# Optimization experiments

Hardware: AMD Instinct MI355X
Metric: run time of the kernel (lower is better)

Reference implementation:

```python
import jax, jax.numpy as jnp
import numpy as np

B, S, DIM = 2, 2048, 2048
H, KVH, HD = 16, 4, 128
WIN = 512
ROPE_BASE = 10000.0
EPS = 1.1920928955078125e-07  # torch F.rms_norm default eps for fp32


def setup_inputs() -> dict:
    key = jax.random.key(0)
    ks = jax.random.split(key, 6)
    kv_dim = KVH * HD
    sc = lambda fan_in: 1.0 / np.sqrt(fan_in)
    return {
        "x": jax.random.normal(ks[0], (B, S, DIM), jnp.float32),
        "Wq": jax.random.normal(ks[1], (DIM, DIM), jnp.float32) * sc(DIM),
        "Wk": jax.random.normal(ks[2], (kv_dim, DIM), jnp.float32) * sc(DIM),
        "Wv": jax.random.normal(ks[3], (kv_dim, DIM), jnp.float32) * sc(DIM),
        "Wo": jax.random.normal(ks[4], (DIM, DIM), jnp.float32) * sc(DIM),
        "q_gain": jnp.ones((H,), jnp.float32),
    }


def _rms_norm(x):
    return x * jax.lax.rsqrt(jnp.mean(x * x, axis=-1, keepdims=True) + EPS)


def _rope_tables(seqlen, dtype):
    half = HD // 2
    inv_freq = ROPE_BASE ** (-jnp.arange(0, half, dtype=jnp.float32) / half)
    freqs = jnp.arange(seqlen, dtype=jnp.float32)[:, None] * inv_freq[None, :]  # [S, HD/2]
    return jnp.cos(freqs).astype(dtype), jnp.sin(freqs).astype(dtype)


def _apply_rotary(x, cos, sin):
    # x: [B, H, S, HD]; cos/sin: [S, HD/2]
    half = x.shape[-1] // 2
    x1, x2 = x[..., :half], x[..., half:]
    c = cos[None, None, :, :]
    s = sin[None, None, :, :]
    return jnp.concatenate([x1 * c + x2 * s, -x1 * s + x2 * c], axis=-1)


def reference(x, Wq, Wk, Wv, Wo, q_gain):
    bsz, seqlen, dim = x.shape
    q = jnp.einsum("bsd,ed->bse", x, Wq).reshape(bsz, seqlen, H, HD).transpose(0, 2, 1, 3)
    k = jnp.einsum("bsd,ed->bse", x, Wk).reshape(bsz, seqlen, KVH, HD).transpose(0, 2, 1, 3)
    v = jnp.einsum("bsd,ed->bse", x, Wv).reshape(bsz, seqlen, KVH, HD).transpose(0, 2, 1, 3)

    q = _rms_norm(q)
    k = _rms_norm(k)

    cos, sin = _rope_tables(seqlen, q.dtype)
    q = _apply_rotary(q, cos, sin)
    k = _apply_rotary(k, cos, sin)

    q = q * q_gain[None, :, None, None]

    # GQA: expand kv heads to match query heads
    rep = H // KVH
    k = jnp.repeat(k, rep, axis=1)
    v = jnp.repeat(v, rep, axis=1)

    row = jnp.arange(seqlen)[:, None]
    col = jnp.arange(seqlen)[None, :]
    mask = (col <= row) & (col >= row - WIN + 1)  # [S, S]

    scale = 1.0 / np.sqrt(HD)
    scores = jnp.einsum("bhsd,bhtd->bhst", q, k) * scale
    scores = jnp.where(mask[None, None, :, :], scores, -jnp.inf)
    attn = jax.nn.softmax(scores, axis=-1)
    y = jnp.einsum("bhst,bhtd->bhsd", attn, v)  # [B, H, S, HD]

    y = y.transpose(0, 2, 1, 3).reshape(bsz, seqlen, dim)
    return jnp.einsum("bsd,ed->bse", y, Wo)
```

## Files before the change

### kernel.cpp

```cpp
#include <hip/hip_runtime.h>

#define S_LEN 2048
#define DIM   2048
#define NH    16
#define NKV   4
#define HD    128
#define WIN   512
#define BATCH 2

typedef __bf16 bf16x8 __attribute__((ext_vector_type(8)));
typedef __bf16 bf16x4 __attribute__((ext_vector_type(4)));
typedef float  f32x4  __attribute__((ext_vector_type(4)));

__device__ inline void async_load16(const void* g, void* l) {
  __builtin_amdgcn_global_load_lds(
      (const __attribute__((address_space(1))) unsigned int*)g,
      (__attribute__((address_space(3))) unsigned int*)l, 16, 0, 0);
}

__global__ __launch_bounds__(256) void rope_tables_kernel(
    float* __restrict__ cosT, float* __restrict__ sinT) {
  int idx = blockIdx.x * 256 + threadIdx.x;
  int s = idx >> 6, d = idx & 63;
  float f = (float)s * powf(10000.f, -(float)d * (1.f / 64.f));
  float sn, cs;
  sincosf(f, &sn, &cs);
  cosT[idx] = cs;
  sinT[idx] = sn;
}

__global__ __launch_bounds__(256) void cast_bf16_kernel(
    const float* __restrict__ in, __bf16* __restrict__ out, int n4) {
  int i = blockIdx.x * 256 + threadIdx.x;
  if (i < n4) {
    float4 v = ((const float4*)in)[i];
    bf16x4 o;
    o[0] = (__bf16)v.x; o[1] = (__bf16)v.y; o[2] = (__bf16)v.z; o[3] = (__bf16)v.w;
    ((bf16x4*)out)[i] = o;
  }
}

__global__ __launch_bounds__(256) void cast_weights_kernel(
    const float* __restrict__ Wq, const float* __restrict__ Wk,
    const float* __restrict__ Wv, const float* __restrict__ Wo,
    __bf16* __restrict__ wqkv, __bf16* __restrict__ wob) {
  int i = blockIdx.x * 256 + threadIdx.x;
  int orow = i >> 9, c = i & 511;
  const float* src;
  __bf16* dst;
  long soff;
  if (orow < 2048) {
    int n = orow & 127;
    int sr = (orow & ~127) + ((n >> 5) << 4) + (n & 15) + (((n >> 4) & 1) << 6);
    src = Wq; soff = (long)sr * 512 + c; dst = wqkv + (long)orow * 2048;
  } else if (orow < 2560) {
    int lr = orow - 2048, n = lr & 127;
    int sr = (lr & ~127) + ((n >> 5) << 4) + (n & 15) + (((n >> 4) & 1) << 6);
    src = Wk; soff = (long)sr * 512 + c; dst = wqkv + (long)orow * 2048;
  } else if (orow < 3072) {
    src = Wv; soff = (long)(orow - 2560) * 512 + c; dst = wqkv + (long)orow * 2048;
  } else {
    src = Wo; soff = (long)(orow - 3072) * 512 + c; dst = wob + (long)(orow - 3072) * 2048;
  }
  float4 v = ((const float4*)src)[soff];
  bf16x4 o;
  o[0] = (__bf16)v.x; o[1] = (__bf16)v.y; o[2] = (__bf16)v.z; o[3] = (__bf16)v.w;
  ((bf16x4*)(dst))[c] = o;
}

__global__ __launch_bounds__(256) void gemm_bt(
    const __bf16* __restrict__ A, const __bf16* __restrict__ Bt,
    float* __restrict__ C, int M, int N, int K) {
  __shared__ __bf16 As[128 * 32];
  __shared__ __bf16 Bs[128 * 32];
  const int t = threadIdx.x;
  const int wid = t >> 6, lane = t & 63;
  const int quad = lane >> 4, l15 = lane & 15;
  const long m0 = (long)blockIdx.x * 128, n0 = (long)blockIdx.y * 128;
  const int wm = (wid >> 1) * 64, wn = (wid & 1) * 64;

  const __bf16* ga = A + (m0 + (t >> 2)) * (long)K + (t & 3) * 8;
  const __bf16* gb = Bt + (n0 + (t >> 2)) * (long)K + (t & 3) * 8;
  char* lA = (char*)As + wid * 1024;
  char* lB = (char*)Bs + wid * 1024;
  const long rstride = 64L * K;

  f32x4 zero = {0.f, 0.f, 0.f, 0.f};
  f32x4 acc[4][4];
#pragma unroll
  for (int i = 0; i < 4; ++i)
#pragma unroll
    for (int j = 0; j < 4; ++j) acc[i][j] = zero;

  for (int k0 = 0; k0 < K; k0 += 32) {
    async_load16(ga + k0, lA);
    async_load16(ga + k0 + rstride, lA + 4096);
    async_load16(gb + k0, lB);
    async_load16(gb + k0 + rstride, lB + 4096);
    __syncthreads();
    bf16x8 af[4], bfr[4];
#pragma unroll
    for (int i = 0; i < 4; ++i) {
      af[i] = *(const bf16x8*)(As + (wm + i * 16 + l15) * 32 + quad * 8);
      bfr[i] = *(const bf16x8*)(Bs + (wn + i * 16 + l15) * 32 + quad * 8);
    }
#pragma unroll
    for (int i = 0; i < 4; ++i)
#pragma unroll
      for (int j = 0; j < 4; ++j)
        acc[i][j] = __builtin_amdgcn_mfma_f32_16x16x32_bf16(af[i], bfr[j], acc[i][j], 0, 0, 0);
    __syncthreads();
  }

#pragma unroll
  for (int i = 0; i < 4; ++i)
#pragma unroll
    for (int j = 0; j < 4; ++j)
#pragma unroll
      for (int r = 0; r < 4; ++r)
        C[(m0 + wm + i * 16 + quad * 4 + r) * (long)N + n0 + wn + j * 16 + l15] = acc[i][j][r];
}

__global__ __launch_bounds__(256) void gemm_qkv(
    const __bf16* __restrict__ A,
    const __bf16* __restrict__ Bt,
    const float* __restrict__ gain,
    const float* __restrict__ cosT, const float* __restrict__ sinT,
    __bf16* __restrict__ Qo,
    __bf16* __restrict__ Ko,
    __bf16* __restrict__ Vt) {
  __shared__ __bf16 As[128 * 32];
  __shared__ __bf16 Bs[128 * 32];
  const int K = 2048;
  const int t = threadIdx.x;
  const int wid = t >> 6, lane = t & 63;
  const int quad = lane >> 4, l15 = lane & 15;
  const long m0 = (long)blockIdx.x * 128, n0 = (long)blockIdx.y * 128;
  const int wm = (wid >> 1) * 64, wn = (wid & 1) * 64;

  const __bf16* ga = A + (m0 + (t >> 2)) * (long)K + (t & 3) * 8;
  const __bf16* gb = Bt + (n0 + (t >> 2)) * (long)K + (t & 3) * 8;
  char* lA = (char*)As + wid * 1024;
  char* lB = (char*)Bs + wid * 1024;
  const long rstride = 64L * K;

  f32x4 zero = {0.f, 0.f, 0.f, 0.f};
  f32x4 acc[4][4];
#pragma unroll
  for (int i = 0; i < 4; ++i)
#pragma unroll
    for (int j = 0; j < 4; ++j) acc[i][j] = zero;

  for (int k0 = 0; k0 < K; k0 += 32) {
    async_load16(ga + k0, lA);
    async_load16(ga + k0 + rstride, lA + 4096);
    async_load16(gb + k0, lB);
    async_load16(gb + k0 + rstride, lB + 4096);
    __syncthreads();
    bf16x8 af[4], bfr[4];
#pragma unroll
    for (int i = 0; i < 4; ++i) {
      af[i] = *(const bf16x8*)(As + (wm + i * 16 + l15) * 32 + quad * 8);
      bfr[i] = *(const bf16x8*)(Bs + (wn + i * 16 + l15) * 32 + quad * 8);
    }
#pragma unroll
    for (int i = 0; i < 4; ++i)
#pragma unroll
      for (int j = 0; j < 4; ++j)
        acc[i][j] = __builtin_amdgcn_mfma_f32_16x16x32_bf16(af[i], bfr[j], acc[i][j], 0, 0, 0);
    __syncthreads();
  }

  const int by = blockIdx.y;
  const int srow0 = (int)(m0 & 2047);
  const int bb = (int)(m0 >> 11);

  if (by >= 20) {
    const int kvh = by - 20;
    __bf16* Vb = Vt + ((long)(bb * NKV + kvh)) * HD * S_LEN;
#pragma unroll
    for (int i = 0; i < 4; ++i)
#pragma unroll
      for (int j = 0; j < 4; ++j) {
        int d = wn + j * 16 + l15;
        int s0 = srow0 + wm + i * 16 + quad * 4;
        bf16x4 o;
#pragma unroll
        for (int r = 0; r < 4; ++r) o[r] = (__bf16)acc[i][j][r];
        *(bf16x4*)(Vb + (long)d * S_LEN + s0) = o;
      }
  } else {
    float* sums = (float*)As;
#pragma unroll
    for (int i = 0; i < 4; ++i)
#pragma unroll
      for (int r = 0; r < 4; ++r) {
        float t2 = acc[i][0][r] * acc[i][0][r] + acc[i][1][r] * acc[i][1][r] +
                   acc[i][2][r] * acc[i][2][r] + acc[i][3][r] * acc[i][3][r];
#pragma unroll
        for (int off = 1; off < 16; off <<= 1) t2 += __shfl_xor(t2, off, 64);
        if (l15 == 0) sums[(wm + i * 16 + quad * 4 + r) * 2 + (wn >> 6)] = t2;
      }
    __syncthreads();

    float g;
    __bf16* base;
    if (by < 16) {
      g = gain[by] * 0.08838834764831845f;
      base = Qo + ((long)(bb * NH + by)) * S_LEN * HD;
    } else {
      g = 1.f;
      base = Ko + ((long)(bb * NKV + (by - 16))) * S_LEN * HD;
    }
#pragma unroll
    for (int i = 0; i < 4; ++i)
#pragma unroll
      for (int r = 0; r < 4; ++r) {
        int lrow = wm + i * 16 + quad * 4 + r;
        int srow = srow0 + lrow;
        float rs = rsqrtf((sums[lrow * 2] + sums[lrow * 2 + 1]) * (1.f / 128.f) +
                          1.1920928955078125e-07f);
#pragma unroll
        for (int a = 0; a < 2; ++a) {
          int dlow = (wn >> 1) + a * 16 + l15;
          float cv = cosT[srow * 64 + dlow];
          float sv = sinT[srow * 64 + dlow];
          float x1 = acc[i][2 * a][r] * rs;
          float x2 = acc[i][2 * a + 1][r] * rs;
          base[(long)srow * HD + wn + (2 * a) * 16 + l15] = (__bf16)((x1 * cv + x2 * sv) * g);
          base[(long)srow * HD + wn + (2 * a + 1) * 16 + l15] = (__bf16)((-x1 * sv + x2 * cv) * g);
        }
      }
  }
}

__global__ __launch_bounds__(128) void attn_kernel(
    const __bf16* __restrict__ Q,
    const __bf16* __restrict__ K,
    const __bf16* __restrict__ Vt,
    const float* __restrict__ gain,
    __bf16* __restrict__ Y) {
  __shared__ __bf16 Ks[64 * 128];
  __shared__ __bf16 Vs[128 * 64];
  __shared__ __bf16 Ps[2][32 * 64];

  const int t = threadIdx.x;
  const int wid = t >> 6, lane = t & 63;
  const int quad = lane >> 4, l15 = lane & 15;
  const int qt = 31 - blockIdx.x;
  const int h = blockIdx.y, b = blockIdx.z;
  const int kv = h >> 2;
  const int t0 = qt * 64;
  const int r0 = t0 + wid * 32;

  const __bf16* Qb = Q + ((long)(b * NH + h)) * S_LEN * HD;
  const __bf16* Kb = K + ((long)(b * NKV + kv)) * S_LEN * HD;
  const __bf16* Vb = Vt + ((long)(b * NKV + kv)) * HD * S_LEN;
  const float M = 11.3137085f * fabsf(gain[h]);

  bf16x8 qf[2][4];
#pragma unroll
  for (int mt = 0; mt < 2; ++mt)
#pragma unroll
    for (int c = 0; c < 4; ++c)
      qf[mt][c] = *(const bf16x8*)(Qb + (long)(r0 + mt * 16 + l15) * HD + c * 32 + quad * 8);

  f32x4 zero = {0.f, 0.f, 0.f, 0.f};
  f32x4 acc[2][8];
#pragma unroll
  for (int mt = 0; mt < 2; ++mt)
#pragma unroll
    for (int d = 0; d < 8; ++d) acc[mt][d] = zero;
  float lac[2][4];
#pragma unroll
  for (int mt = 0; mt < 2; ++mt)
#pragma unroll
    for (int r = 0; r < 4; ++r) lac[mt][r] = 0.f;

  int koff[8], voff[8];
#pragma unroll
  for (int jj = 0; jj < 8; ++jj) {
    int kr = wid * 32 + jj * 4 + (lane >> 4);
    koff[jj] = kr * HD + (((lane & 15) ^ (kr & 7)) << 3);
    int vr = wid * 64 + jj * 8 + (lane >> 3);
    voff[jj] = vr * S_LEN + (((lane & 7) ^ (vr & 7)) << 3);
  }

  const int kstart = (t0 >= WIN) ? (t0 - WIN) : 0;
  const int ntiles = (t0 + 64 - kstart) >> 6;

  for (int it = 0; it < ntiles; ++it) {
    const int kt = kstart + it * 64;
#pragma unroll
    for (int jj = 0; jj < 8; ++jj) {
      async_load16(Kb + (long)kt * HD + koff[jj], (char*)Ks + wid * 8192 + jj * 1024);
      async_load16(Vb + kt + voff[jj], (char*)Vs + wid * 8192 + jj * 1024);
    }
    __syncthreads();

    if (kt <= r0 + 31 && kt + 63 >= r0 - (WIN - 1)) {
      f32x4 sc[2][4];
#pragma unroll
      for (int nt = 0; nt < 4; ++nt) { sc[0][nt] = zero; sc[1][nt] = zero; }
#pragma unroll
      for (int nt = 0; nt < 4; ++nt)
#pragma unroll
        for (int c = 0; c < 4; ++c) {
          bf16x8 kf = *(const bf16x8*)(Ks + (nt * 16 + l15) * 128 +
                                       (((c * 4 + quad) ^ (l15 & 7)) << 3));
          sc[0][nt] = __builtin_amdgcn_mfma_f32_16x16x32_bf16(qf[0][c], kf, sc[0][nt], 0, 0, 0);
          sc[1][nt] = __builtin_amdgcn_mfma_f32_16x16x32_bf16(qf[1][c], kf, sc[1][nt], 0, 0, 0);
        }
#pragma unroll
      for (int mt = 0; mt < 2; ++mt)
#pragma unroll
        for (int r = 0; r < 4; ++r) {
          const int prow = mt * 16 + quad * 4 + r;
          const int row = r0 + prow;
#pragma unroll
          for (int nt = 0; nt < 4; ++nt) {
            const int key = kt + nt * 16 + l15;
            float p = (key <= row && key >= row - (WIN - 1))
                          ? __expf(sc[mt][nt][r] - M) : 0.f;
            lac[mt][r] += p;
            int chunk = nt * 2 + (l15 >> 3);
            Ps[wid][prow * 64 + ((chunk ^ (prow & 7)) << 3) + (l15 & 7)] = (__bf16)p;
          }
        }
      bf16x8 pf[2][2];
#pragma unroll
      for (int mt = 0; mt < 2; ++mt)
#pragma unroll
        for (int kc = 0; kc < 2; ++kc)
          pf[mt][kc] = *(const bf16x8*)(&Ps[wid][(mt * 16 + l15) * 64 +
                                                 (((kc * 4 + quad) ^ (l15 & 7)) << 3)]);
#pragma unroll
      for (int dt = 0; dt < 8; ++dt)
#pragma unroll
        for (int kc = 0; kc < 2; ++kc) {
          bf16x8 vf = *(const bf16x8*)(Vs + (dt * 16 + l15) * 64 +
                                       (((kc * 4 + quad) ^ (l15 & 7)) << 3));
          acc[0][dt] = __builtin_amdgcn_mfma_f32_16x16x32_bf16(pf[0][kc], vf, acc[0][dt], 0, 0, 0);
          acc[1][dt] = __builtin_amdgcn_mfma_f32_16x16x32_bf16(pf[1][kc], vf, acc[1][dt], 0, 0, 0);
        }
    }
    __syncthreads();
  }

  __bf16* Yb = Y + ((long)b * S_LEN) * DIM + h * HD;
#pragma unroll
  for (int mt = 0; mt < 2; ++mt)
#pragma unroll
    for (int r = 0; r < 4; ++r) {
      float ls = lac[mt][r];
#pragma unroll
      for (int off = 1; off < 16; off <<= 1) ls += __shfl_xor(ls, off, 64);
      float il = 1.f / ls;
#pragma unroll
      for (int d = 0; d < 8; ++d)
        Yb[(long)(r0 + mt * 16 + quad * 4 + r) * DIM + d * 16 + l15] =
            (__bf16)(acc[mt][d][r] * il);
    }
}

extern "C" void kernel_launch(void* const* d_in, const int* in_sizes, int n_in,
                              void* d_out, int out_size, void* d_ws, size_t ws_size,
                              hipStream_t stream) {
  (void)in_sizes; (void)n_in; (void)out_size; (void)ws_size;
  const float* x  = (const float*)d_in[0];
  const float* Wq = (const float*)d_in[1];
  const float* Wk = (const float*)d_in[2];
  const float* Wv = (const float*)d_in[3];
  const float* Wo = (const float*)d_in[4];
  const float* qg = (const float*)d_in[5];
  float* out = (float*)d_out;

  char* ws = (char*)d_ws;
  size_t off = 0;
  auto alloc = [&](size_t bytes) -> void* {
    void* p = ws + off;
    off += (bytes + 255) & ~(size_t)255;
    return p;
  };
  __bf16* xb   = (__bf16*)alloc(8388608ull * 2);
  __bf16* wqkv = (__bf16*)alloc(3072ull * 2048 * 2);
  __bf16* wob  = (__bf16*)alloc(2048ull * 2048 * 2);
  __bf16* qo   = (__bf16*)alloc((size_t)BATCH * NH * S_LEN * HD * 2);
  __bf16* ko   = (__bf16*)alloc((size_t)BATCH * NKV * S_LEN * HD * 2);
  __bf16* vt   = (__bf16*)alloc((size_t)BATCH * NKV * HD * S_LEN * 2);
  float*  cosT = (float*)alloc(2048ull * 64 * 4);
  float*  sinT = (float*)alloc(2048ull * 64 * 4);
  __bf16* yb   = xb;

  rope_tables_kernel<<<512, 256, 0, stream>>>(cosT, sinT);
  cast_bf16_kernel<<<8192, 256, 0, stream>>>(x, xb, 8388608 / 4);
  cast_weights_kernel<<<10240, 256, 0, stream>>>(Wq, Wk, Wv, Wo, wqkv, wob);

  gemm_qkv<<<dim3(32, 24), 256, 0, stream>>>(xb, wqkv, qg, cosT, sinT, qo, ko, vt);
  attn_kernel<<<dim3(32, 16, 2), 128, 0, stream>>>(qo, ko, vt, qg, yb);
  gemm_bt<<<dim3(32, 16), 256, 0, stream>>>(yb, wob, out, 4096, 2048, 2048);
}
```

Baseline: 283.9 us.

## Double-buffer GEMM and attention tiles, fuse preprocessing kernels, enlarge attention query tiles

Folds the three preprocessing kernels (x cast, weight cast and permute, rope tables) into one launch. Both GEMMs now use double-buffered LDS, prefetching the next K slice while computing the current one, with one barrier per iteration instead of two. The attention kernel is restructured to 128-query blocks with 64 rows per wave and 32-key double-buffered K/V tiles. It computes transposed scores so P is written as bf16x4 chunks, with new swizzles and row sums reduced through LDS. The larger per-wave accumulators raise register pressure, and the attention grid is halved.

```diff
diff --git a/kernel.cpp b/kernel.cpp
--- a/kernel.cpp
+++ b/kernel.cpp
@@ -12,67 +12,66 @@
 typedef __bf16 bf16x4 __attribute__((ext_vector_type(4)));
 typedef float  f32x4  __attribute__((ext_vector_type(4)));
 
+union U8 { bf16x8 v; bf16x4 h[2]; };
+
 __device__ inline void async_load16(const void* g, void* l) {
   __builtin_amdgcn_global_load_lds(
       (const __attribute__((address_space(1))) unsigned int*)g,
       (__attribute__((address_space(3))) unsigned int*)l, 16, 0, 0);
 }
 
-__global__ __launch_bounds__(256) void rope_tables_kernel(
+__global__ __launch_bounds__(256) void preprocess_kernel(
+    const float* __restrict__ x,
+    const float* __restrict__ Wq, const float* __restrict__ Wk,
+    const float* __restrict__ Wv, const float* __restrict__ Wo,
+    __bf16* __restrict__ xb, __bf16* __restrict__ wqkv, __bf16* __restrict__ wob,
     float* __restrict__ cosT, float* __restrict__ sinT) {
-  int idx = blockIdx.x * 256 + threadIdx.x;
-  int s = idx >> 6, d = idx & 63;
-  float f = (float)s * powf(10000.f, -(float)d * (1.f / 64.f));
-  float sn, cs;
-  sincosf(f, &sn, &cs);
-  cosT[idx] = cs;
-  sinT[idx] = sn;
-}
-
-__global__ __launch_bounds__(256) void cast_bf16_kernel(
-    const float* __restrict__ in, __bf16* __restrict__ out, int n4) {
-  int i = blockIdx.x * 256 + threadIdx.x;
-  if (i < n4) {
-    float4 v = ((const float4*)in)[i];
+  const int blk = blockIdx.x, tid = threadIdx.x;
+  if (blk < 8192) {
+    int i = blk * 256 + tid;
+    float4 v = ((const float4*)x)[i];
     bf16x4 o;
     o[0] = (__bf16)v.x; o[1] = (__bf16)v.y; o[2] = (__bf16)v.z; o[3] = (__bf16)v.w;
-    ((bf16x4*)out)[i] = o;
-  }
-}
-
-__global__ __launch_bounds__(256) void cast_weights_kernel(
-    const float* __restrict__ Wq, const float* __restrict__ Wk,
-    const float* __restrict__ Wv, const float* __restrict__ Wo,
-    __bf16* __restrict__ wqkv, __bf16* __restrict__ wob) {
-  int i = blockIdx.x * 256 + threadIdx.x;
-  int orow = i >> 9, c = i & 511;
-  const float* src;
-  __bf16* dst;
-  long soff;
-  if (orow < 2048) {
-    int n = orow & 127;
-    int sr = (orow & ~127) + ((n >> 5) << 4) + (n & 15) + (((n >> 4) & 1) << 6);
-    src = Wq; soff = (long)sr * 512 + c; dst = wqkv + (long)orow * 2048;
-  } else if (orow < 2560) {
-    int lr = orow - 2048, n = lr & 127;
-    int sr = (lr & ~127) + ((n >> 5) << 4) + (n & 15) + (((n >> 4) & 1) << 6);
-    src = Wk; soff = (long)sr * 512 + c; dst = wqkv + (long)orow * 2048;
-  } else if (orow < 3072) {
-    src = Wv; soff = (long)(orow - 2560) * 512 + c; dst = wqkv + (long)orow * 2048;
+    ((bf16x4*)xb)[i] = o;
+  } else if (blk < 18432) {
+    int i = (blk - 8192) * 256 + tid;
+    int orow = i >> 9, c = i & 511;
+    const float* src;
+    __bf16* dst;
+    long soff;
+    if (orow < 2048) {
+      int n = orow & 127;
+      int sr = (orow & ~127) + ((n >> 5) << 4) + (n & 15) + (((n >> 4) & 1) << 6);
+      src = Wq; soff = (long)sr * 512 + c; dst = wqkv + (long)orow * 2048;
+    } else if (orow < 2560) {
+      int lr = orow - 2048, n = lr & 127;
+      int sr = (lr & ~127) + ((n >> 5) << 4) + (n & 15) + (((n >> 4) & 1) << 6);
+      src = Wk; soff = (long)sr * 512 + c; dst = wqkv + (long)orow * 2048;
+    } else if (orow < 3072) {
+      src = Wv; soff = (long)(orow - 2560) * 512 + c; dst = wqkv + (long)orow * 2048;
+    } else {
+      src = Wo; soff = (long)(orow - 3072) * 512 + c; dst = wob + (long)(orow - 3072) * 2048;
+    }
+    float4 v = ((const float4*)src)[soff];
+    bf16x4 o;
+    o[0] = (__bf16)v.x; o[1] = (__bf16)v.y; o[2] = (__bf16)v.z; o[3] = (__bf16)v.w;
+    ((bf16x4*)dst)[c] = o;
   } else {
-    src = Wo; soff = (long)(orow - 3072) * 512 + c; dst = wob + (long)(orow - 3072) * 2048;
-  }
-  float4 v = ((const float4*)src)[soff];
-  bf16x4 o;
-  o[0] = (__bf16)v.x; o[1] = (__bf16)v.y; o[2] = (__bf16)v.z; o[3] = (__bf16)v.w;
-  ((bf16x4*)(dst))[c] = o;
+    int idx = (blk - 18432) * 256 + tid;
+    int s = idx >> 6, d = idx & 63;
+    float f = (float)s * powf(10000.f, -(float)d * (1.f / 64.f));
+    float sn, cs;
+    sincosf(f, &sn, &cs);
+    cosT[idx] = cs;
+    sinT[idx] = sn;
+  }
 }
 
 __global__ __launch_bounds__(256) void gemm_bt(
     const __bf16* __restrict__ A, const __bf16* __restrict__ Bt,
     float* __restrict__ C, int M, int N, int K) {
-  __shared__ __bf16 As[128 * 32];
-  __shared__ __bf16 Bs[128 * 32];
+  __shared__ __bf16 As[2][128 * 32];
+  __shared__ __bf16 Bs[2][128 * 32];
   const int t = threadIdx.x;
   const int wid = t >> 6, lane = t & 63;
   const int quad = lane >> 4, l15 = lane & 15;
@@ -81,8 +80,6 @@
 
   const __bf16* ga = A + (m0 + (t >> 2)) * (long)K + (t & 3) * 8;
   const __bf16* gb = Bt + (n0 + (t >> 2)) * (long)K + (t & 3) * 8;
-  char* lA = (char*)As + wid * 1024;
-  char* lB = (char*)Bs + wid * 1024;
   const long rstride = 64L * K;
 
   f32x4 zero = {0.f, 0.f, 0.f, 0.f};
@@ -92,24 +89,35 @@
 #pragma unroll
     for (int j = 0; j < 4; ++j) acc[i][j] = zero;
 
-  for (int k0 = 0; k0 < K; k0 += 32) {
-    async_load16(ga + k0, lA);
-    async_load16(ga + k0 + rstride, lA + 4096);
-    async_load16(gb + k0, lB);
-    async_load16(gb + k0 + rstride, lB + 4096);
+  async_load16(ga, (char*)As[0] + wid * 1024);
+  async_load16(ga + rstride, (char*)As[0] + 4096 + wid * 1024);
+  async_load16(gb, (char*)Bs[0] + wid * 1024);
+  async_load16(gb + rstride, (char*)Bs[0] + 4096 + wid * 1024);
+
+  const int niter = K >> 5;
+  for (int it = 0; it < niter; ++it) {
     __syncthreads();
+    if (it + 1 < niter) {
+      const int kn = (it + 1) << 5;
+      const int nb = (it + 1) & 1;
+      async_load16(ga + kn, (char*)As[nb] + wid * 1024);
+      async_load16(ga + kn + rstride, (char*)As[nb] + 4096 + wid * 1024);
+      async_load16(gb + kn, (char*)Bs[nb] + wid * 1024);
+      async_load16(gb + kn + rstride, (char*)Bs[nb] + 4096 + wid * 1024);
+    }
+    const __bf16* as = As[it & 1];
+    const __bf16* bs = Bs[it & 1];
     bf16x8 af[4], bfr[4];
 #pragma unroll
     for (int i = 0; i < 4; ++i) {
-      af[i] = *(const bf16x8*)(As + (wm + i * 16 + l15) * 32 + quad * 8);
-      bfr[i] = *(const bf16x8*)(Bs + (wn + i * 16 + l15) * 32 + quad * 8);
+      af[i] = *(const bf16x8*)(as + (wm + i * 16 + l15) * 32 + quad * 8);
+      bfr[i] = *(const bf16x8*)(bs + (wn + i * 16 + l15) * 32 + quad * 8);
     }
 #pragma unroll
     for (int i = 0; i < 4; ++i)
 #pragma unroll
       for (int j = 0; j < 4; ++j)
         acc[i][j] = __builtin_amdgcn_mfma_f32_16x16x32_bf16(af[i], bfr[j], acc[i][j], 0, 0, 0);
-    __syncthreads();
   }
 
 #pragma unroll
@@ -122,15 +130,12 @@
 }
 
 __global__ __launch_bounds__(256) void gemm_qkv(
-    const __bf16* __restrict__ A,
-    const __bf16* __restrict__ Bt,
+    const __bf16* __restrict__ A, const __bf16* __restrict__ Bt,
     const float* __restrict__ gain,
     const float* __restrict__ cosT, const float* __restrict__ sinT,
-    __bf16* __restrict__ Qo,
-    __bf16* __restrict__ Ko,
-    __bf16* __restrict__ Vt) {
-  __shared__ __bf16 As[128 * 32];
-  __shared__ __bf16 Bs[128 * 32];
+    __bf16* __restrict__ Qo, __bf16* __restrict__ Ko, __bf16* __restrict__ Vt) {
+  __shared__ __bf16 As[2][128 * 32];
+  __shared__ __bf16 Bs[2][128 * 32];
   const int K = 2048;
   const int t = threadIdx.x;
   const int wid = t >> 6, lane = t & 63;
@@ -140,8 +145,6 @@
 
   const __bf16* ga = A + (m0 + (t >> 2)) * (long)K + (t & 3) * 8;
   const __bf16* gb = Bt + (n0 + (t >> 2)) * (long)K + (t & 3) * 8;
-  char* lA = (char*)As + wid * 1024;
-  char* lB = (char*)Bs + wid * 1024;
   const long rstride = 64L * K;
 
   f32x4 zero = {0.f, 0.f, 0.f, 0.f};
@@ -151,24 +154,35 @@
 #pragma unroll
     for (int j = 0; j < 4; ++j) acc[i][j] = zero;
 
-  for (int k0 = 0; k0 < K; k0 += 32) {
-    async_load16(ga + k0, lA);
-    async_load16(ga + k0 + rstride, lA + 4096);
-    async_load16(gb + k0, lB);
-    async_load16(gb + k0 + rstride, lB + 4096);
+  async_load16(ga, (char*)As[0] + wid * 1024);
+  async_load16(ga + rstride, (char*)As[0] + 4096 + wid * 1024);
+  async_load16(gb, (char*)Bs[0] + wid * 1024);
+  async_load16(gb + rstride, (char*)Bs[0] + 4096 + wid * 1024);
+
+  const int niter = K >> 5;
+  for (int it = 0; it < niter; ++it) {
     __syncthreads();
+    if (it + 1 < niter) {
+      const int kn = (it + 1) << 5;
+      const int nb = (it + 1) & 1;
+      async_load16(ga + kn, (char*)As[nb] + wid * 1024);
+      async_load16(ga + kn + rstride, (char*)As[nb] + 4096 + wid * 1024);
+      async_load16(gb + kn, (char*)Bs[nb] + wid * 1024);
+      async_load16(gb + kn + rstride, (char*)Bs[nb] + 4096 + wid * 1024);
+    }
+    const __bf16* as = As[it & 1];
+    const __bf16* bs = Bs[it & 1];
     bf16x8 af[4], bfr[4];
 #pragma unroll
     for (int i = 0; i < 4; ++i) {
-      af[i] = *(const bf16x8*)(As + (wm + i * 16 + l15) * 32 + quad * 8);
-      bfr[i] = *(const bf16x8*)(Bs + (wn + i * 16 + l15) * 32 + quad * 8);
+      af[i] = *(const bf16x8*)(as + (wm + i * 16 + l15) * 32 + quad * 8);
+      bfr[i] = *(const bf16x8*)(bs + (wn + i * 16 + l15) * 32 + quad * 8);
     }
 #pragma unroll
     for (int i = 0; i < 4; ++i)
 #pragma unroll
       for (int j = 0; j < 4; ++j)
         acc[i][j] = __builtin_amdgcn_mfma_f32_16x16x32_bf16(af[i], bfr[j], acc[i][j], 0, 0, 0);
-    __syncthreads();
   }
 
   const int by = blockIdx.y;
@@ -234,132 +248,146 @@
   }
 }
 
-__global__ __launch_bounds__(128) void attn_kernel(
+__global__ __launch_bounds__(128, 1) void attn_kernel(
     const __bf16* __restrict__ Q,
     const __bf16* __restrict__ K,
     const __bf16* __restrict__ Vt,
     const float* __restrict__ gain,
     __bf16* __restrict__ Y) {
-  __shared__ __bf16 Ks[64 * 128];
-  __shared__ __bf16 Vs[128 * 64];
-  __shared__ __bf16 Ps[2][32 * 64];
+  __shared__ __bf16 Ks[2][32 * 128];
+  __shared__ __bf16 Vs[2][128 * 32];
+  __shared__ __bf16 Ps[2][64 * 32];
+  __shared__ float  Ls[2][64];
 
   const int t = threadIdx.x;
   const int wid = t >> 6, lane = t & 63;
   const int quad = lane >> 4, l15 = lane & 15;
-  const int qt = 31 - blockIdx.x;
+  const int qt_blk = 15 - blockIdx.x;
   const int h = blockIdx.y, b = blockIdx.z;
   const int kv = h >> 2;
-  const int t0 = qt * 64;
-  const int r0 = t0 + wid * 32;
+  const int t0 = qt_blk * 128;
+  const int r0 = t0 + wid * 64;
 
   const __bf16* Qb = Q + ((long)(b * NH + h)) * S_LEN * HD;
   const __bf16* Kb = K + ((long)(b * NKV + kv)) * S_LEN * HD;
   const __bf16* Vb = Vt + ((long)(b * NKV + kv)) * HD * S_LEN;
   const float M = 11.3137085f * fabsf(gain[h]);
 
-  bf16x8 qf[2][4];
-#pragma unroll
-  for (int mt = 0; mt < 2; ++mt)
+  bf16x8 qf[4][4];
+#pragma unroll
+  for (int qt = 0; qt < 4; ++qt)
 #pragma unroll
     for (int c = 0; c < 4; ++c)
-      qf[mt][c] = *(const bf16x8*)(Qb + (long)(r0 + mt * 16 + l15) * HD + c * 32 + quad * 8);
+      qf[qt][c] = *(const bf16x8*)(Qb + (long)(r0 + qt * 16 + l15) * HD + c * 32 + quad * 8);
 
   f32x4 zero = {0.f, 0.f, 0.f, 0.f};
-  f32x4 acc[2][8];
-#pragma unroll
-  for (int mt = 0; mt < 2; ++mt)
+  f32x4 acc[4][8];
+#pragma unroll
+  for (int mt = 0; mt < 4; ++mt)
 #pragma unroll
     for (int d = 0; d < 8; ++d) acc[mt][d] = zero;
-  float lac[2][4];
-#pragma unroll
-  for (int mt = 0; mt < 2; ++mt)
-#pragma unroll
-    for (int r = 0; r < 4; ++r) lac[mt][r] = 0.f;
-
-  int koff[8], voff[8];
-#pragma unroll
-  for (int jj = 0; jj < 8; ++jj) {
-    int kr = wid * 32 + jj * 4 + (lane >> 4);
-    koff[jj] = kr * HD + (((lane & 15) ^ (kr & 7)) << 3);
-    int vr = wid * 64 + jj * 8 + (lane >> 3);
-    voff[jj] = vr * S_LEN + (((lane & 7) ^ (vr & 7)) << 3);
+  float lac[4] = {0.f, 0.f, 0.f, 0.f};
+
+  int ksrc[4], vsrc[4];
+#pragma unroll
+  for (int j = 0; j < 4; ++j) {
+    int kr = j * 8 + (t >> 4);
+    ksrc[j] = kr * HD + (((t & 15) ^ (kr & 15)) << 3);
+    int vd = j * 32 + (t >> 2);
+    vsrc[j] = vd * S_LEN + (((t & 3) ^ (vd & 3)) << 3);
   }
 
   const int kstart = (t0 >= WIN) ? (t0 - WIN) : 0;
-  const int ntiles = (t0 + 64 - kstart) >> 6;
+  const int ntiles = (t0 + 128 - kstart) >> 5;
+
+#pragma unroll
+  for (int j = 0; j < 4; ++j) {
+    async_load16(Kb + (long)kstart * HD + ksrc[j], (char*)Ks[0] + j * 2048 + wid * 1024);
+    async_load16(Vb + kstart + vsrc[j], (char*)Vs[0] + j * 2048 + wid * 1024);
+  }
 
   for (int it = 0; it < ntiles; ++it) {
-    const int kt = kstart + it * 64;
-#pragma unroll
-    for (int jj = 0; jj < 8; ++jj) {
-      async_load16(Kb + (long)kt * HD + koff[jj], (char*)Ks + wid * 8192 + jj * 1024);
-      async_load16(Vb + kt + voff[jj], (char*)Vs + wid * 8192 + jj * 1024);
-    }
+    const int kt = kstart + it * 32;
     __syncthreads();
-
-    if (kt <= r0 + 31 && kt + 63 >= r0 - (WIN - 1)) {
-      f32x4 sc[2][4];
-#pragma unroll
-      for (int nt = 0; nt < 4; ++nt) { sc[0][nt] = zero; sc[1][nt] = zero; }
-#pragma unroll
-      for (int nt = 0; nt < 4; ++nt)
-#pragma unroll
-        for (int c = 0; c < 4; ++c) {
-          bf16x8 kf = *(const bf16x8*)(Ks + (nt * 16 + l15) * 128 +
-                                       (((c * 4 + quad) ^ (l15 & 7)) << 3));
-          sc[0][nt] = __builtin_amdgcn_mfma_f32_16x16x32_bf16(qf[0][c], kf, sc[0][nt], 0, 0, 0);
-          sc[1][nt] = __builtin_amdgcn_mfma_f32_16x16x32_bf16(qf[1][c], kf, sc[1][nt], 0, 0, 0);
+    if (it + 1 < ntiles) {
+      const int kn = kt + 32;
+      const int nb = (it + 1) & 1;
+#pragma unroll
+      for (int j = 0; j < 4; ++j) {
+        async_load16(Kb + (long)kn * HD + ksrc[j], (char*)Ks[nb] + j * 2048 + wid * 1024);
+        async_load16(Vb + kn + vsrc[j], (char*)Vs[nb] + j * 2048 + wid * 1024);
+      }
+    }
+    if (kt <= r0 + 63 && kt + 31 >= r0 - (WIN - 1)) {
+      const __bf16* ksb = Ks[it & 1];
+      const __bf16* vsb = Vs[it & 1];
+#pragma unroll
+      for (int kti = 0; kti < 2; ++kti) {
+        bf16x8 kf[4];
+#pragma unroll
+        for (int c = 0; c < 4; ++c)
+          kf[c] = *(const bf16x8*)(ksb + (kti * 16 + l15) * 128 +
+                                   ((((c << 2) + quad) ^ l15) << 3));
+#pragma unroll
+        for (int qt = 0; qt < 4; ++qt) {
+          f32x4 sc = zero;
+#pragma unroll
+          for (int c = 0; c < 4; ++c)
+            sc = __builtin_amdgcn_mfma_f32_16x16x32_bf16(kf[c], qf[qt][c], sc, 0, 0, 0);
+          const int q = qt * 16 + l15;
+          const int qg = r0 + q;
+          const int kbase = kt + kti * 16 + quad * 4;
+          bf16x4 pv;
+#pragma unroll
+          for (int r = 0; r < 4; ++r) {
+            int key = kbase + r;
+            float p = (key <= qg && key >= qg - (WIN - 1)) ? __expf(sc[r] - M) : 0.f;
+            lac[qt] += p;
+            pv[r] = (__bf16)p;
+          }
+          const int sw = (q + (q >> 3)) & 7;
+          const int cb = kti * 4 + quad;
+          *(bf16x4*)(&Ps[wid][q * 32 + ((cb ^ sw) << 2)]) = pv;
         }
-#pragma unroll
-      for (int mt = 0; mt < 2; ++mt)
-#pragma unroll
-        for (int r = 0; r < 4; ++r) {
-          const int prow = mt * 16 + quad * 4 + r;
-          const int row = r0 + prow;
-#pragma unroll
-          for (int nt = 0; nt < 4; ++nt) {
-            const int key = kt + nt * 16 + l15;
-            float p = (key <= row && key >= row - (WIN - 1))
-                          ? __expf(sc[mt][nt][r] - M) : 0.f;
-            lac[mt][r] += p;
-            int chunk = nt * 2 + (l15 >> 3);
-            Ps[wid][prow * 64 + ((chunk ^ (prow & 7)) << 3) + (l15 & 7)] = (__bf16)p;
-          }
-        }
-      bf16x8 pf[2][2];
-#pragma unroll
-      for (int mt = 0; mt < 2; ++mt)
-#pragma unroll
-        for (int kc = 0; kc < 2; ++kc)
-          pf[mt][kc] = *(const bf16x8*)(&Ps[wid][(mt * 16 + l15) * 64 +
-                                                 (((kc * 4 + quad) ^ (l15 & 7)) << 3)]);
+      }
+      bf16x8 pf[4];
+#pragma unroll
+      for (int mt = 0; mt < 4; ++mt) {
+        const int q = mt * 16 + l15;
+        const int sw = (q + (q >> 3)) & 7;
+        U8 u;
+        u.h[0] = *(const bf16x4*)(&Ps[wid][q * 32 + (((2 * quad) ^ sw) << 2)]);
+        u.h[1] = *(const bf16x4*)(&Ps[wid][q * 32 + (((2 * quad + 1) ^ sw) << 2)]);
+        pf[mt] = u.v;
+      }
+#pragma unroll
+      for (int dt = 0; dt < 8; ++dt) {
+        bf16x8 vf = *(const bf16x8*)(vsb + (dt * 16 + l15) * 32 +
+                                     ((quad ^ (l15 & 3)) << 3));
+#pragma unroll
+        for (int mt = 0; mt < 4; ++mt)
+          acc[mt][dt] = __builtin_amdgcn_mfma_f32_16x16x32_bf16(pf[mt], vf, acc[mt][dt], 0, 0, 0);
+      }
+    }
+  }
+
+#pragma unroll
+  for (int qt = 0; qt < 4; ++qt) {
+    float s = lac[qt];
+    s += __shfl_xor(s, 16, 64);
+    s += __shfl_xor(s, 32, 64);
+    if (quad == 0) Ls[wid][qt * 16 + l15] = s;
+  }
+  __bf16* Yb = Y + ((long)b * S_LEN) * DIM + h * HD;
+#pragma unroll
+  for (int mt = 0; mt < 4; ++mt)
+#pragma unroll
+    for (int r = 0; r < 4; ++r) {
+      float il = 1.f / Ls[wid][mt * 16 + quad * 4 + r];
+      const long row = r0 + mt * 16 + quad * 4 + r;
 #pragma unroll
       for (int dt = 0; dt < 8; ++dt)
-#pragma unroll
-        for (int kc = 0; kc < 2; ++kc) {
-          bf16x8 vf = *(const bf16x8*)(Vs + (dt * 16 + l15) * 64 +
-                                       (((kc * 4 + quad) ^ (l15 & 7)) << 3));
-          acc[0][dt] = __builtin_amdgcn_mfma_f32_16x16x32_bf16(pf[0][kc], vf, acc[0][dt], 0, 0, 0);
-          acc[1][dt] = __builtin_amdgcn_mfma_f32_16x16x32_bf16(pf[1][kc], vf, acc[1][dt], 0, 0, 0);
-        }
-    }
-    __syncthreads();
-  }
-
-  __bf16* Yb = Y + ((long)b * S_LEN) * DIM + h * HD;
-#pragma unroll
-  for (int mt = 0; mt < 2; ++mt)
-#pragma unroll
-    for (int r = 0; r < 4; ++r) {
-      float ls = lac[mt][r];
-#pragma unroll
-      for (int off = 1; off < 16; off <<= 1) ls += __shfl_xor(ls, off, 64);
-      float il = 1.f / ls;
-#pragma unroll
-      for (int d = 0; d < 8; ++d)
-        Yb[(long)(r0 + mt * 16 + quad * 4 + r) * DIM + d * 16 + l15] =
-            (__bf16)(acc[mt][d][r] * il);
+        Yb[row * DIM + dt * 16 + l15] = (__bf16)(acc[mt][dt][r] * il);
     }
 }
 
@@ -392,11 +420,9 @@
   float*  sinT = (float*)alloc(2048ull * 64 * 4);
   __bf16* yb   = xb;
 
-  rope_tables_kernel<<<512, 256, 0, stream>>>(cosT, sinT);
-  cast_bf16_kernel<<<8192, 256, 0, stream>>>(x, xb, 8388608 / 4);
-  cast_weights_kernel<<<10240, 256, 0, stream>>>(Wq, Wk, Wv, Wo, wqkv, wob);
-
+  preprocess_kernel<<<18944, 256, 0, stream>>>(x, Wq, Wk, Wv, Wo, xb, wqkv, wob,
+                                               cosT, sinT);
   gemm_qkv<<<dim3(32, 24), 256, 0, stream>>>(xb, wqkv, qg, cosT, sinT, qo, ko, vt);
-  attn_kernel<<<dim3(32, 16, 2), 128, 0, stream>>>(qo, ko, vt, qg, yb);
+  attn_kernel<<<dim3(16, 16, 2), 128, 0, stream>>>(qo, ko, vt, qg, yb);
   gemm_bt<<<dim3(32, 16), 256, 0, stream>>>(yb, wob, out, 4096, 2048, 2048);
 }
```

Measured after the change: 320.9 us. 13.0% more time.
